# Optimization experiments

Hardware: AMD Instinct MI355X
Metric: run time of the kernel (lower is better)

The kernel has to match this reference:

```python
import jax, jax.numpy as jnp
import numpy as np

# Config (from ModelConfig in source; num_layers reduced to 4 for the reference)
B, T, D = 4, 8192, 1024
P = 512            # num_patches
S = 4              # patch_stride (OverlapAddDecoder upsample factor)
L = 4              # num transformer layers
NH, NKV, HD = 16, 4, 64
FF = 4096          # ffn_multiplier * D
KC = 256           # MoD capacity = 0.5 * P
V = 257            # vocab_size


def rmsnorm(x, w, eps=1e-6):
    return x * jax.lax.rsqrt(jnp.mean(x * x, -1, keepdims=True) + eps) * w


def rope_cache(n, d):
    theta = 1.0 / (10000.0 ** (jnp.arange(0, d, 2, dtype=jnp.float32) / d))
    fr = jnp.arange(n, dtype=jnp.float32)[:, None] * theta[None, :]
    e = jnp.concatenate([fr, fr], -1)
    return jnp.cos(e), jnp.sin(e)  # (n, d) each


def rot_half(x):
    h = x.shape[-1] // 2
    return jnp.concatenate([-x[..., h:], x[..., :h]], -1)


def setup_inputs() -> dict:
    key = jax.random.key(0)
    ks = iter(jax.random.split(key, 40))
    n = lambda s: jax.random.normal(next(ks), s, dtype=jnp.float32) * 0.02
    return {
        'tokens': jax.random.randint(next(ks), (B, T), 0, V),
        'emb': n((V, D)),
        'bp_w1': n((D // 2, D, 3)), 'bp_b1': jnp.zeros((D // 2,), jnp.float32),
        'bp_w2': n((1, D // 2, 3)), 'bp_b2': jnp.zeros((1,), jnp.float32),
        'enc_norm_w': jnp.ones((D,), jnp.float32),
        'router_w': n((L, D)),
        'ln1_w': jnp.ones((L, D), jnp.float32), 'ln2_w': jnp.ones((L, D), jnp.float32),
        'q_w': n((L, D, D)), 'k_w': n((L, D, NKV * HD)), 'v_w': n((L, D, NKV * HD)), 'o_w': n((L, D, D)),
        'gate_w': n((L, D, FF)), 'up_w': n((L, D, FF)), 'down_w': n((L, FF, D)),
        'dec_proj_w': n((D, S * D)), 'dec_proj_b': jnp.zeros((S * D,), jnp.float32),
        'dec_mlp_w1': n((D, D // 4)), 'dec_mlp_b1': jnp.zeros((D // 4,), jnp.float32),
        'dec_mlp_w2': n((D // 4, S)), 'dec_mlp_b2': jnp.zeros((S,), jnp.float32),
        'dec_norm_w': jnp.ones((D,), jnp.float32),
        'head_w': n((D, V)),
    }


def reference(tokens, emb, bp_w1, bp_b1, bp_w2, bp_b2, enc_norm_w, router_w,
              ln1_w, ln2_w, q_w, k_w, v_w, o_w, gate_w, up_w, down_w,
              dec_proj_w, dec_proj_b, dec_mlp_w1, dec_mlp_b1, dec_mlp_w2, dec_mlp_b2,
              dec_norm_w, head_w):
    x = emb[tokens]  # (B, T, D) byte embeddings

    # --- LearnedBoundaryPredictor: 2-layer 1D CNN -> per-segment soft boundaries ---
    dn = ('NCH', 'OIH', 'NCH')
    xT = x.transpose(0, 2, 1)  # (B, D, T)
    h1 = jax.lax.conv_general_dilated(xT, bp_w1, (1,), ((1, 1),), dimension_numbers=dn) + bp_b1[None, :, None]
    h1 = jax.nn.gelu(h1)
    lg = jax.lax.conv_general_dilated(h1, bp_w2, (1,), ((1, 1),), dimension_numbers=dn) + bp_b2[None, :, None]
    lg = lg[:, 0, :]  # (B, T)

    seg = T // P  # uniform segments (T divisible by P so all segments equal)
    lgw = jax.nn.softmax(lg.reshape(B, P, seg), -1)
    pos = jnp.arange(T, dtype=jnp.float32).reshape(P, seg)
    bp = jnp.sum(lgw * pos[None], -1)                                   # (B, P) soft boundary positions
    ent = -jnp.sum(lgw * jnp.log(jnp.clip(lgw, 1e-8)), -1) / np.log(seg)  # (B, P) entropy signal

    # --- gather patch embeddings at boundary positions, RMSNorm ---
    idx = jnp.clip(bp.astype(jnp.int32), 0, T - 1)
    patches = jnp.take_along_axis(x, idx[..., None], 1)  # (B, P, D)
    xp = rmsnorm(patches, enc_norm_w)

    cos, sin = rope_cache(P, HD)
    b_idx = jnp.arange(B)[:, None]
    causal = jnp.tril(jnp.ones((KC, KC), bool))
    G = NH // NKV

    # --- MoD-routed transformer stack: top-k tokens go through the layer ---
    for l in range(L):
        rl = jnp.einsum('bpd,d->bp', xp, router_w[l]) + ent  # router logits (entropy-boosted)
        _, sel = jax.lax.top_k(rl, KC)
        sel = jnp.sort(sel, -1)  # ascending positions -> causal order preserved
        xs = xp[b_idx, sel]      # (B, KC, D) selected tokens
        g = jax.nn.sigmoid(rl[b_idx, sel])[..., None]  # router gate
        cs = cos[sel][:, None]   # (B, 1, KC, HD)
        sn = sin[sel][:, None]

        # GQA with RoPE, causal
        h = rmsnorm(xs, ln1_w[l])
        q = (h @ q_w[l]).reshape(B, KC, NH, HD).transpose(0, 2, 1, 3)
        k = (h @ k_w[l]).reshape(B, KC, NKV, HD).transpose(0, 2, 1, 3)
        v = (h @ v_w[l]).reshape(B, KC, NKV, HD).transpose(0, 2, 1, 3)
        q = q * cs + rot_half(q) * sn
        k = k * cs + rot_half(k) * sn
        k = jnp.repeat(k, G, axis=1)
        v = jnp.repeat(v, G, axis=1)
        sc = jnp.einsum('bhqd,bhkd->bhqk', q, k) / np.sqrt(HD)
        sc = jnp.where(causal, sc, -1e30)
        a = jax.nn.softmax(sc, -1)
        ao = (jnp.einsum('bhqk,bhkd->bhqd', a, v).transpose(0, 2, 1, 3).reshape(B, KC, D)) @ o_w[l]

        x2 = xs + ao
        h2 = rmsnorm(x2, ln2_w[l])
        ff = (jax.nn.silu(h2 @ gate_w[l]) * (h2 @ up_w[l])) @ down_w[l]
        delta = ao + ff  # layer(x_sel) - x_sel
        xp = xp.at[b_idx, sel].add(g * delta)  # scatter back; unselected pass through

    # --- OverlapAddDecoder ---
    proj = (xp @ dec_proj_w + dec_proj_b).reshape(B, P, S, D)
    win = jax.nn.sigmoid(jax.nn.gelu(xp @ dec_mlp_w1 + dec_mlp_b1) @ dec_mlp_w2 + dec_mlp_b2)  # (B, P, S)
    out = rmsnorm((proj * win[..., None]).reshape(B, P * S, D), dec_norm_w)
    return out @ head_w  # (B, P*S, V) byte logits
```

## Files before the change

### kernel.cpp

```cpp
#include <hip/hip_runtime.h>
#include <hip/hip_bf16.h>
#include <math.h>

constexpr int Bn  = 4;
constexpr int Tn  = 8192;
constexpr int Dn  = 1024;
constexpr int Pn  = 512;
constexpr int SEGn= 16;
constexpr int Sn  = 4;
constexpr int Ln  = 4;
constexpr int NHn = 16;
constexpr int NKVn= 4;
constexpr int HDn = 64;
constexpr int FFn = 4096;
constexpr int KCn = 256;
constexpr int Vn  = 257;
constexpr int DHn = 512;

constexpr long OFF_EW  = 0;
constexpr long OFF_CA  = 394752;
constexpr long OFF_CB  = 427520;
constexpr long OFF_CC  = 460288;
constexpr long OFF_ENT = 493056;
constexpr long OFF_IDX = 495104;
constexpr long OFF_XP  = 497152;
constexpr long OFF_RL  = 2594304;
constexpr long OFF_SEL = 2596352;
constexpr long OFF_G   = 2597376;
constexpr long SCR     = 2598400;
constexpr long SC_XS   = 0;
constexpr long SC_H    = 1048576;
constexpr long SC_Q    = 2097152;
constexpr long SC_KV   = 3145728;
constexpr long SC_AOUT = 3670016;
constexpr long SC_AO   = 4718592;
constexpr long SC_H2   = 5767168;
constexpr long SC_GU   = 6815744;
constexpr long SC_FF   = 15204352;
constexpr long SC_PROJ = 0;
constexpr long SC_HMLP = 8388608;
constexpr long SC_WIN  = 8912896;
constexpr long SC_Y    = 8921088;
constexpr long SC_EA   = 0;
constexpr long SC_WB   = 524288;
constexpr long OFF_WT    = 19908096;
constexpr long OFF_PARTS = 24102400;
constexpr long OFF_GHL   = 28820992;

typedef __attribute__((ext_vector_type(8))) short short8;
typedef __attribute__((ext_vector_type(4))) float floatx4;

__device__ __forceinline__ float geluf(float x) {
    float u = 0.7978845608028654f * (x + 0.044715f * x * x * x);
    float e = __expf(2.f * u);
    float t = 1.f - 2.f / (e + 1.f);
    return 0.5f * x * (1.f + t);
}
__device__ __forceinline__ float sigmf(float x) { return 1.f / (1.f + expf(-x)); }

__device__ __forceinline__ void cvt_hilo(float x, unsigned short& h, unsigned short& l) {
    unsigned u = __float_as_uint(x);
    h = (unsigned short)(u >> 16);
    float r = x - __uint_as_float(u & 0xffff0000u);
    l = (unsigned short)(__float_as_uint(r) >> 16);
}

typedef const __attribute__((address_space(1))) unsigned int* gas_p;
typedef __attribute__((address_space(3))) unsigned int* las_p;
__device__ __forceinline__ void gload16(const unsigned short* g, unsigned short* l) {
    __builtin_amdgcn_global_load_lds((gas_p)g, (las_p)l, 16, 0, 0);
}

__device__ __forceinline__ float blk_sum256(float v, float* red) {
    for (int o = 32; o > 0; o >>= 1) v += __shfl_down(v, o);
    int lane = threadIdx.x & 63, w = threadIdx.x >> 6;
    if (lane == 0) red[w] = v;
    __syncthreads();
    float r = red[0] + red[1] + red[2] + red[3];
    __syncthreads();
    return r;
}

__global__ void k_emb_pad(const float* __restrict__ emb, unsigned short* __restrict__ EA) {
    int i = blockIdx.x * blockDim.x + threadIdx.x;
    if (i >= 384 * 1024) return;
    int r = i >> 10, d = i & 1023;
    float v = (r < Vn) ? emb[r * 1024 + d] : 0.f;
    unsigned short hh, ll;
    cvt_hilo(v, hh, ll);
    EA[(long)r * 2048 + d] = hh;
    EA[(long)r * 2048 + 1024 + d] = ll;
}

__global__ void k_wconv_w1(const float* __restrict__ w1, unsigned short* __restrict__ WB) {
    int i = blockIdx.x * blockDim.x + threadIdx.x;
    if (i >= 1536 * 1024) return;
    int n = i >> 10, k = i & 1023;
    float v = w1[(n / 3) * 3072 + k * 3 + (n % 3)];
    unsigned short hh, ll;
    cvt_hilo(v, hh, ll);
    WB[(long)n * 2048 + k] = hh;
    WB[(long)n * 2048 + 1024 + k] = ll;
}

__global__ void k_ewred(const float* __restrict__ parts, float* __restrict__ EW) {
    int i = blockIdx.x * blockDim.x + threadIdx.x;
    if (i >= 3 * Vn * DHn) return;
    int dk = i / (Vn * DHn);
    int rem = i - dk * (Vn * DHn);
    int v = rem >> 9, o = rem & 511;
    long src = (long)v * 1536 + o * 3 + dk;
    float s = 0.f;
    constexpr long MN = 384L * 1536;
    #pragma unroll
    for (int c = 0; c < 4; c++) s += parts[c * MN + src];
    EW[i] = s;
}

__global__ void k_conv1(const int* __restrict__ tok, const float* __restrict__ EW,
                        const float* __restrict__ b1, const float* __restrict__ w2,
                        float* __restrict__ cA, float* __restrict__ cB, float* __restrict__ cC) {
    int wave = threadIdx.x >> 6, lane = threadIdx.x & 63;
    int gidx = blockIdx.x * 4 + wave;
    int b = gidx / Tn, t = gidx - b * Tn;
    int tk  = tok[b * Tn + t];
    int tkm = (t > 0)      ? tok[b * Tn + t - 1] : -1;
    int tkp = (t < Tn - 1) ? tok[b * Tn + t + 1] : -1;
    const float* E0 = EW;
    const float* E1 = EW + (long)Vn * DHn;
    const float* E2 = EW + 2L * Vn * DHn;
    float a0 = 0.f, a1 = 0.f, a2 = 0.f;
    #pragma unroll
    for (int u = 0; u < DHn / 64; u++) {
        int o = lane + u * 64;
        float s = b1[o] + E1[tk * DHn + o];
        if (tkm >= 0) s += E0[tkm * DHn + o];
        if (tkp >= 0) s += E2[tkp * DHn + o];
        float hg = geluf(s);
        a0 += hg * w2[o * 3 + 0];
        a1 += hg * w2[o * 3 + 1];
        a2 += hg * w2[o * 3 + 2];
    }
    for (int o = 32; o > 0; o >>= 1) {
        a0 += __shfl_down(a0, o); a1 += __shfl_down(a1, o); a2 += __shfl_down(a2, o);
    }
    if (lane == 0) { cA[gidx] = a0; cB[gidx] = a1; cC[gidx] = a2; }
}

__global__ void k_patchstats(const float* __restrict__ cA, const float* __restrict__ cB,
                             const float* __restrict__ cC, const float* __restrict__ b2,
                             float* __restrict__ ent_out, int* __restrict__ idx_out) {
    int pid = blockIdx.x * blockDim.x + threadIdx.x;
    if (pid >= Bn * Pn) return;
    int b = pid / Pn, p = pid - b * Pn;
    float lgv[SEGn];
    float m = -3.4e38f;
    for (int s = 0; s < SEGn; s++) {
        int t = p * SEGn + s;
        float v = b2[0] + cB[b * Tn + t];
        if (t > 0)      v += cA[b * Tn + t - 1];
        if (t < Tn - 1) v += cC[b * Tn + t + 1];
        lgv[s] = v; m = fmaxf(m, v);
    }
    float Z = 0.f;
    for (int s = 0; s < SEGn; s++) { lgv[s] = expf(lgv[s] - m); Z += lgv[s]; }
    float inv = 1.f / Z;
    float bp = 0.f, en = 0.f;
    for (int s = 0; s < SEGn; s++) {
        float w = lgv[s] * inv;
        bp += w * (float)(p * SEGn + s);
        en -= w * logf(fmaxf(w, 1e-8f));
    }
    en *= (1.f / 2.772588722239781f);
    ent_out[pid] = en;
    int ix = (int)bp;
    ix = ix < 0 ? 0 : (ix > Tn - 1 ? Tn - 1 : ix);
    idx_out[pid] = ix;
}

__global__ void k_xp(const int* __restrict__ tok, const int* __restrict__ idx,
                     const float* __restrict__ emb, const float* __restrict__ nw,
                     float* __restrict__ xp) {
    int pid = blockIdx.x;
    int b = pid / Pn;
    int tk = tok[b * Tn + idx[pid]];
    const float* row = emb + (long)tk * Dn;
    __shared__ float red[4];
    float v[4]; float ss = 0.f;
    #pragma unroll
    for (int j = 0; j < 4; j++) { v[j] = row[threadIdx.x + j * 256]; ss += v[j] * v[j]; }
    ss = blk_sum256(ss, red);
    float sc = 1.f / sqrtf(ss * (1.f / Dn) + 1e-6f);
    #pragma unroll
    for (int j = 0; j < 4; j++) {
        int d = threadIdx.x + j * 256;
        xp[(long)pid * Dn + d] = v[j] * sc * nw[d];
    }
}

__global__ void k_router(const float* __restrict__ xp, const float* __restrict__ rw,
                         const float* __restrict__ ent, float* __restrict__ rl) {
    int pid = blockIdx.x;
    const float* xr = xp + (long)pid * Dn;
    __shared__ float red[4];
    float s = 0.f;
    #pragma unroll
    for (int j = 0; j < 4; j++) { int d = threadIdx.x + j * 256; s += xr[d] * rw[d]; }
    s = blk_sum256(s, red);
    if (threadIdx.x == 0) rl[pid] = s + ent[pid];
}

__global__ void k_topk(const float* __restrict__ rl, int* __restrict__ sel, float* __restrict__ g) {
    int b = blockIdx.x, p = threadIdx.x;
    __shared__ float vals[Pn];
    __shared__ int flag[Pn];
    float v = rl[b * Pn + p];
    vals[p] = v;
    __syncthreads();
    int rank = 0;
    for (int q = 0; q < Pn; q++) {
        float vq = vals[q];
        rank += (vq > v || (vq == v && q < p)) ? 1 : 0;
    }
    int selected = rank < KCn ? 1 : 0;
    flag[p] = selected;
    __syncthreads();
    if (selected) {
        int pos = 0;
        for (int q = 0; q < p; q++) pos += flag[q];
        sel[b * KCn + pos] = p;
        g[b * KCn + pos] = sigmf(v);
    }
}

__global__ void k_gather_ln1(const float* __restrict__ xp, const int* __restrict__ sel,
                             const float* __restrict__ w, float* __restrict__ xs,
                             unsigned short* __restrict__ hHL) {
    int r = blockIdx.x;
    int b = r / KCn;
    int p = sel[r];
    const float* src = xp + ((long)b * Pn + p) * Dn;
    __shared__ float red[4];
    float v[4]; float ss = 0.f;
    #pragma unroll
    for (int j = 0; j < 4; j++) { v[j] = src[threadIdx.x + j * 256]; ss += v[j] * v[j]; }
    ss = blk_sum256(ss, red);
    float sc = 1.f / sqrtf(ss * (1.f / Dn) + 1e-6f);
    #pragma unroll
    for (int j = 0; j < 4; j++) {
        int d = threadIdx.x + j * 256;
        xs[(long)r * Dn + d] = v[j];
        unsigned short hh, ll;
        cvt_hilo(v[j] * sc * w[d], hh, ll);
        hHL[(long)r * 2048 + d] = hh;
        hHL[(long)r * 2048 + 1024 + d] = ll;
    }
}

__global__ void k_wconv(const float* __restrict__ Wm, unsigned short* __restrict__ Whl,
                        int K, int N) {
    __shared__ float t[32][33];
    int n0 = blockIdx.x * 32, k0 = blockIdx.y * 32;
    int tx = threadIdx.x & 31, ty = threadIdx.x >> 5;
    #pragma unroll
    for (int r = 0; r < 4; r++) {
        int k = k0 + ty + 8 * r, n = n0 + tx;
        t[ty + 8 * r][tx] = (n < N) ? Wm[(long)k * N + n] : 0.f;
    }
    __syncthreads();
    long K2 = 2L * K;
    #pragma unroll
    for (int r = 0; r < 4; r++) {
        int n = n0 + ty + 8 * r, k = k0 + tx;
        float v = t[tx][ty + 8 * r];
        unsigned short hh, ll;
        cvt_hilo(v, hh, ll);
        Whl[(long)n * K2 + k] = hh;
        Whl[(long)n * K2 + K + k] = ll;
    }
}

__global__ void k_xcvt(const float* __restrict__ src, unsigned short* __restrict__ dhl, int n) {
    int i = blockIdx.x * blockDim.x + threadIdx.x;
    if (i >= n) return;
    int r = i >> 10, d = i & 1023;
    unsigned short hh, ll;
    cvt_hilo(src[i], hh, ll);
    dhl[(long)r * 2048 + d] = hh;
    dhl[(long)r * 2048 + 1024 + d] = ll;
}

__global__ __launch_bounds__(256, 2) void k_mfma3(
        const unsigned short* __restrict__ Ag, const unsigned short* __restrict__ Bg,
        float* __restrict__ Cmat, const float* __restrict__ bias,
        int M, int N, int K, int splitK, float* __restrict__ parts) {
    __shared__ alignas(16) unsigned short As[2][128 * 64], Bs[2][128 * 64];
    int tid = threadIdx.x;
    int m0 = blockIdx.y * 128, n0 = blockIdx.x * 128;
    int kc = blockIdx.z;
    int Kc = K / splitK, kbase = kc * Kc, KT = Kc >> 5;
    int lane = tid & 63, wid = tid >> 6;
    int wm = (wid & 1) * 64, wn = (wid >> 1) * 64;
    int quad = lane >> 4, l16 = lane & 15;

    int srow8 = lane >> 3;
    int spos  = lane & 7;
    int cch   = spos ^ srow8;
    long K2 = 2L * K;
    long coff = (cch < 4) ? (long)(cch * 8) : (long)K + (long)((cch - 4) * 8);
    const unsigned short* Aseg = Ag + (long)(m0 + srow8) * K2 + coff;
    const unsigned short* Bseg = Bg + (long)(n0 + srow8) * K2 + coff;

    floatx4 acc[4][4];
    #pragma unroll
    for (int i = 0; i < 4; i++)
        #pragma unroll
        for (int j = 0; j < 4; j++) acc[i][j] = (floatx4){0.f, 0.f, 0.f, 0.f};

    auto stagef = [&](unsigned short* Ad, unsigned short* Bd, long kb) {
        #pragma unroll
        for (int t = 0; t < 4; t++) {
            int sa = wid * 4 + t;
            gload16(Aseg + (long)sa * 8 * K2 + kb, Ad + sa * 512);
            gload16(Bseg + (long)sa * 8 * K2 + kb, Bd + sa * 512);
        }
    };

    int ph = quad ^ (l16 & 7);
    stagef(As[0], Bs[0], kbase);
    __syncthreads();
    int cur = 0;
    for (int ks = 0; ks < KT; ks++) {
        if (ks + 1 < KT)
            stagef(As[cur ^ 1], Bs[cur ^ 1], kbase + (long)(ks + 1) * 32);

        const unsigned short* Ac = As[cur];
        const unsigned short* Bc = Bs[cur];
        short8 ah[4], al2[4], bh[4], bl2[4];
        #pragma unroll
        for (int i = 0; i < 4; i++) {
            int r = wm + i * 16 + l16;
            ah[i]  = *(const short8*)&Ac[r * 64 + ph * 8];
            al2[i] = *(const short8*)&Ac[r * 64 + (ph ^ 4) * 8];
        }
        #pragma unroll
        for (int j = 0; j < 4; j++) {
            int c = wn + j * 16 + l16;
            bh[j]  = *(const short8*)&Bc[c * 64 + ph * 8];
            bl2[j] = *(const short8*)&Bc[c * 64 + (ph ^ 4) * 8];
        }
        #pragma unroll
        for (int i = 0; i < 4; i++)
            #pragma unroll
            for (int j = 0; j < 4; j++) {
                acc[i][j] = __builtin_amdgcn_mfma_f32_16x16x32_bf16(ah[i],  bh[j],  acc[i][j], 0, 0, 0);
                acc[i][j] = __builtin_amdgcn_mfma_f32_16x16x32_bf16(ah[i],  bl2[j], acc[i][j], 0, 0, 0);
                acc[i][j] = __builtin_amdgcn_mfma_f32_16x16x32_bf16(al2[i], bh[j],  acc[i][j], 0, 0, 0);
            }
        __syncthreads();
        cur ^= 1;
    }

    long MN = (long)M * N;
    #pragma unroll
    for (int j = 0; j < 4; j++) {
        int n = n0 + wn + j * 16 + l16;
        if (n >= N) continue;
        float bvx = bias ? bias[n] : 0.f;
        #pragma unroll
        for (int i = 0; i < 4; i++) {
            int mb = m0 + wm + i * 16 + quad * 4;
            #pragma unroll
            for (int r = 0; r < 4; r++) {
                if (splitK > 1) parts[kc * MN + (long)(mb + r) * N + n] = acc[i][j][r];
                else            Cmat[(long)(mb + r) * N + n] = acc[i][j][r] + bvx;
            }
        }
    }
}

__global__ void k_reduce(const float* __restrict__ parts, float* __restrict__ out,
                         const float* __restrict__ bias, long MN, int sk, int N) {
    long i = (long)blockIdx.x * blockDim.x + threadIdx.x;
    if (i >= MN) return;
    float s = 0.f;
    for (int c = 0; c < sk; c++) s += parts[c * MN + i];
    if (bias) s += bias[(int)(i % N)];
    out[i] = s;
}

__global__ void k_rope(float* __restrict__ buf, const int* __restrict__ sel, int nh, int stride) {
    int tid = blockIdx.x * blockDim.x + threadIdx.x;
    int total = Bn * KCn * nh * 32;
    if (tid >= total) return;
    int d = tid & 31;
    int h = (tid >> 5) % nh;
    int r = tid / (32 * nh);
    int pos = sel[r];
    float theta = powf(10000.f, -(float)(2 * d) / 64.f);
    float ang = (float)pos * theta;
    float c = cosf(ang), s = sinf(ang);
    long base = (long)r * stride + h * 64 + d;
    float x1 = buf[base], x2 = buf[base + 32];
    buf[base]      = x1 * c - x2 * s;
    buf[base + 32] = x2 * c + x1 * s;
}

constexpr int APS = 72;
__global__ __launch_bounds__(256) void k_attn(const float* __restrict__ q, const float* __restrict__ kv,
                       unsigned short* __restrict__ aoHL) {
    int bx = blockIdx.x, h = blockIdx.y, b = blockIdx.z;
    int hk = h >> 2;
    int qb0 = bx * 64;
    int tid = threadIdx.x, lane = tid & 63, wid = tid >> 6;
    int quad = lane >> 4, l16 = lane & 15;
    __shared__ alignas(16) unsigned short LdsA[9216], LdsB[9216];
    unsigned short* Kh = LdsA;          unsigned short* Kl = LdsB;
    unsigned short* Ph = LdsA;          unsigned short* Pl = LdsB;
    unsigned short* Vth = LdsA + 4608;  unsigned short* Vtl = LdsB + 4608;

    int qrow = qb0 + wid * 16 + l16;
    short8 qh[2], ql[2];
    #pragma unroll
    for (int ks = 0; ks < 2; ks++) {
        const float* qp = q + ((long)(b * KCn + qrow)) * (NHn * HDn) + h * HDn + ks * 32 + quad * 8;
        float tmp[8];
        *(float4*)tmp = *(const float4*)qp;
        *(float4*)(tmp + 4) = *(const float4*)(qp + 4);
        #pragma unroll
        for (int j = 0; j < 8; j++) {
            unsigned short hh, ll;
            cvt_hilo(tmp[j], hh, ll);
            qh[ks][j] = (short)hh; ql[ks][j] = (short)ll;
        }
    }

    floatx4 sacc[16];
    #pragma unroll
    for (int t = 0; t < 16; t++) sacc[t] = (floatx4){0.f, 0.f, 0.f, 0.f};

    int qmax = qb0 + 63;
    int nkc = qmax / 128 + 1;
    for (int kc = 0; kc < nkc; kc++) {
        __syncthreads();
        {
            int r = tid >> 1, dh = (tid & 1) * 32;
            const float* kp = kv + ((long)(b * KCn + kc * 128 + r)) * 512 + hk * HDn + dh;
            #pragma unroll
            for (int f = 0; f < 8; f++) {
                float tmp[4];
                *(float4*)tmp = *(const float4*)(kp + f * 4);
                unsigned short h0, h1, h2, h3, l0, l1, l2, l3;
                cvt_hilo(tmp[0], h0, l0); cvt_hilo(tmp[1], h1, l1);
                cvt_hilo(tmp[2], h2, l2); cvt_hilo(tmp[3], h3, l3);
                *(ushort4*)&Kh[r * APS + dh + f * 4] = make_ushort4(h0, h1, h2, h3);
                *(ushort4*)&Kl[r * APS + dh + f * 4] = make_ushort4(l0, l1, l2, l3);
            }
        }
        __syncthreads();
        #pragma unroll
        for (int tj = 0; tj < 8; tj++) {
            int kr = tj * 16 + l16;
            int gt = kc * 8 + tj;
            #pragma unroll
            for (int ks = 0; ks < 2; ks++) {
                short8 bh0 = *(const short8*)&Kh[kr * APS + ks * 32 + quad * 8];
                short8 bl0 = *(const short8*)&Kl[kr * APS + ks * 32 + quad * 8];
                sacc[gt] = __builtin_amdgcn_mfma_f32_16x16x32_bf16(qh[ks], bh0, sacc[gt], 0, 0, 0);
                sacc[gt] = __builtin_amdgcn_mfma_f32_16x16x32_bf16(qh[ks], bl0, sacc[gt], 0, 0, 0);
                sacc[gt] = __builtin_amdgcn_mfma_f32_16x16x32_bf16(ql[ks], bh0, sacc[gt], 0, 0, 0);
            }
        }
    }

    float rowinv[4];
    #pragma unroll
    for (int r = 0; r < 4; r++) {
        int qg = qb0 + wid * 16 + quad * 4 + r;
        float mm = -3.4e38f;
        #pragma unroll
        for (int t = 0; t < 16; t++) {
            int key = t * 16 + l16;
            float s = (key <= qg) ? sacc[t][r] * 0.125f : -1e30f;
            sacc[t][r] = s;
            mm = fmaxf(mm, s);
        }
        #pragma unroll
        for (int o = 1; o < 16; o <<= 1) mm = fmaxf(mm, __shfl_xor(mm, o));
        float zz = 0.f;
        #pragma unroll
        for (int t = 0; t < 16; t++) {
            float e = expf(sacc[t][r] - mm);
            sacc[t][r] = e; zz += e;
        }
        #pragma unroll
        for (int o = 1; o < 16; o <<= 1) zz += __shfl_xor(zz, o);
        rowinv[r] = 1.f / zz;
    }

    floatx4 oacc[4];
    #pragma unroll
    for (int dt = 0; dt < 4; dt++) oacc[dt] = (floatx4){0.f, 0.f, 0.f, 0.f};
    int npv = qmax / 64 + 1;
    for (int c4 = 0; c4 < npv; c4++) {
        __syncthreads();
        {
            #pragma unroll
            for (int it = 0; it < 4; it++) {
                int task = tid + 256 * it;
                int kloc = task & 63, d4 = (task >> 6) * 4;
                float tmp[4];
                *(float4*)tmp = *(const float4*)(kv + ((long)(b * KCn + c4 * 64 + kloc)) * 512 + 256 + hk * HDn + d4);
                #pragma unroll
                for (int i = 0; i < 4; i++) {
                    unsigned short hh, ll;
                    cvt_hilo(tmp[i], hh, ll);
                    Vth[(d4 + i) * APS + kloc] = hh;
                    Vtl[(d4 + i) * APS + kloc] = ll;
                }
            }
        }
        #pragma unroll
        for (int tt = 0; tt < 4; tt++) {
            int t = c4 * 4 + tt;
            #pragma unroll
            for (int r = 0; r < 4; r++) {
                int row = wid * 16 + quad * 4 + r;
                float pv2 = sacc[t][r] * rowinv[r];
                unsigned short hh, ll;
                cvt_hilo(pv2, hh, ll);
                Ph[row * APS + tt * 16 + l16] = hh;
                Pl[row * APS + tt * 16 + l16] = ll;
            }
        }
        __syncthreads();
        short8 pah[2], pal[2];
        #pragma unroll
        for (int ks = 0; ks < 2; ks++) {
            pah[ks] = *(const short8*)&Ph[(wid * 16 + l16) * APS + ks * 32 + quad * 8];
            pal[ks] = *(const short8*)&Pl[(wid * 16 + l16) * APS + ks * 32 + quad * 8];
        }
        #pragma unroll
        for (int dt = 0; dt < 4; dt++) {
            #pragma unroll
            for (int ks = 0; ks < 2; ks++) {
                short8 vbh = *(const short8*)&Vth[(dt * 16 + l16) * APS + ks * 32 + quad * 8];
                short8 vbl = *(const short8*)&Vtl[(dt * 16 + l16) * APS + ks * 32 + quad * 8];
                oacc[dt] = __builtin_amdgcn_mfma_f32_16x16x32_bf16(pah[ks], vbh, oacc[dt], 0, 0, 0);
                oacc[dt] = __builtin_amdgcn_mfma_f32_16x16x32_bf16(pah[ks], vbl, oacc[dt], 0, 0, 0);
                oacc[dt] = __builtin_amdgcn_mfma_f32_16x16x32_bf16(pal[ks], vbh, oacc[dt], 0, 0, 0);
            }
        }
    }

    #pragma unroll
    for (int dt = 0; dt < 4; dt++) {
        #pragma unroll
        for (int r = 0; r < 4; r++) {
            int row = qb0 + wid * 16 + quad * 4 + r;
            long base = ((long)(b * KCn + row)) * 2048 + h * HDn + dt * 16 + l16;
            unsigned short hh, ll;
            cvt_hilo(oacc[dt][r], hh, ll);
            aoHL[base] = hh; aoHL[base + 1024] = ll;
        }
    }
}

__global__ void k_add_ln2(const float* __restrict__ xs, const float* __restrict__ ao,
                          const float* __restrict__ w, unsigned short* __restrict__ h2HL) {
    int r = blockIdx.x;
    __shared__ float red[4];
    float v[4]; float ss = 0.f;
    #pragma unroll
    for (int j = 0; j < 4; j++) {
        int d = threadIdx.x + j * 256;
        float x = xs[(long)r * Dn + d] + ao[(long)r * Dn + d];
        v[j] = x; ss += x * x;
    }
    ss = blk_sum256(ss, red);
    float sc = 1.f / sqrtf(ss * (1.f / Dn) + 1e-6f);
    #pragma unroll
    for (int j = 0; j < 4; j++) {
        int d = threadIdx.x + j * 256;
        unsigned short hh, ll;
        cvt_hilo(v[j] * sc * w[d], hh, ll);
        h2HL[(long)r * 2048 + d] = hh;
        h2HL[(long)r * 2048 + 1024 + d] = ll;
    }
}

__global__ void k_silu_mul(const float* __restrict__ C, unsigned short* __restrict__ ghl, int n) {
    int i = blockIdx.x * blockDim.x + threadIdx.x;
    if (i < n) {
        int r = i >> 12, c = i & 4095;
        float x = C[(long)r * 8192 + c];
        float u = C[(long)r * 8192 + 4096 + c];
        unsigned short hh, ll;
        cvt_hilo(x * sigmf(x) * u, hh, ll);
        ghl[(long)r * 8192 + c] = hh;
        ghl[(long)r * 8192 + 4096 + c] = ll;
    }
}

__global__ void k_scatter(float* __restrict__ xp, const float* __restrict__ ao,
                          const float* __restrict__ ff, const float* __restrict__ g,
                          const int* __restrict__ sel) {
    int r = blockIdx.x;
    int b = r / KCn;
    int p = sel[r];
    float gg = g[r];
    float* dst = xp + ((long)b * Pn + p) * Dn;
    #pragma unroll
    for (int j = 0; j < 4; j++) {
        int d = threadIdx.x + j * 256;
        dst[d] += gg * (ao[(long)r * Dn + d] + ff[(long)r * Dn + d]);
    }
}

__global__ void k_win(const float* __restrict__ hmlp, const float* __restrict__ w2,
                      const float* __restrict__ b2, float* __restrict__ win) {
    int tid = blockIdx.x * blockDim.x + threadIdx.x;
    if (tid >= Bn * Pn * Sn) return;
    int s = tid & 3; int r = tid >> 2;
    float acc = b2[s];
    const float* hr = hmlp + (long)r * 256;
    for (int i = 0; i < 256; i++) acc += geluf(hr[i]) * w2[i * 4 + s];
    win[tid] = sigmf(acc);
}

__global__ void k_dec_norm(const float* __restrict__ proj, const float* __restrict__ win,
                           const float* __restrict__ w, unsigned short* __restrict__ yHL) {
    int r = blockIdx.x;
    float wv = win[r];
    __shared__ float red[4];
    float v[4]; float ss = 0.f;
    #pragma unroll
    for (int j = 0; j < 4; j++) {
        int d = threadIdx.x + j * 256;
        float x = proj[(long)r * Dn + d] * wv;
        v[j] = x; ss += x * x;
    }
    ss = blk_sum256(ss, red);
    float sc = 1.f / sqrtf(ss * (1.f / Dn) + 1e-6f);
    #pragma unroll
    for (int j = 0; j < 4; j++) {
        int d = threadIdx.x + j * 256;
        unsigned short hh, ll;
        cvt_hilo(v[j] * sc * w[d], hh, ll);
        yHL[(long)r * 2048 + d] = hh;
        yHL[(long)r * 2048 + 1024 + d] = ll;
    }
}

extern "C" void kernel_launch(void* const* d_in, const int* in_sizes, int n_in,
                              void* d_out, int out_size, void* d_ws, size_t ws_size,
                              hipStream_t stream) {
    const int*   tokens     = (const int*)  d_in[0];
    const float* emb        = (const float*)d_in[1];
    const float* bp_w1      = (const float*)d_in[2];
    const float* bp_b1      = (const float*)d_in[3];
    const float* bp_w2      = (const float*)d_in[4];
    const float* bp_b2      = (const float*)d_in[5];
    const float* enc_norm_w = (const float*)d_in[6];
    const float* router_w   = (const float*)d_in[7];
    const float* ln1_w      = (const float*)d_in[8];
    const float* ln2_w      = (const float*)d_in[9];
    const float* q_w        = (const float*)d_in[10];
    const float* k_w        = (const float*)d_in[11];
    const float* v_w        = (const float*)d_in[12];
    const float* o_w        = (const float*)d_in[13];
    const float* gate_w     = (const float*)d_in[14];
    const float* up_w       = (const float*)d_in[15];
    const float* down_w     = (const float*)d_in[16];
    const float* dec_proj_w = (const float*)d_in[17];
    const float* dec_proj_b = (const float*)d_in[18];
    const float* dec_mlp_w1 = (const float*)d_in[19];
    const float* dec_mlp_b1 = (const float*)d_in[20];
    const float* dec_mlp_w2 = (const float*)d_in[21];
    const float* dec_mlp_b2 = (const float*)d_in[22];
    const float* dec_norm_w = (const float*)d_in[23];
    const float* head_w     = (const float*)d_in[24];
    float* out = (float*)d_out;

    float* W = (float*)d_ws;
    float* EW   = W + OFF_EW;
    float* cA   = W + OFF_CA;
    float* cB   = W + OFF_CB;
    float* cC   = W + OFF_CC;
    float* ent  = W + OFF_ENT;
    int*   idxb = (int*)(W + OFF_IDX);
    float* xp   = W + OFF_XP;
    float* rl   = W + OFF_RL;
    int*   sel  = (int*)(W + OFF_SEL);
    float* g    = W + OFF_G;
    float* scr  = W + SCR;
    float* xs   = scr + SC_XS;
    unsigned short* hHL   = (unsigned short*)(scr + SC_H);
    float* qb   = scr + SC_Q;
    float* kvb  = scr + SC_KV;
    unsigned short* aoutHL = (unsigned short*)(scr + SC_AOUT);
    float* ao   = scr + SC_AO;
    unsigned short* h2HL  = (unsigned short*)(scr + SC_H2);
    float* gupC = scr + SC_GU;
    float* ffb  = scr + SC_FF;
    float* proj = scr + SC_PROJ;
    float* hmlp = scr + SC_HMLP;
    float* win  = scr + SC_WIN;
    unsigned short* yHL   = (unsigned short*)(scr + SC_Y);
    unsigned short* EA    = (unsigned short*)(scr + SC_EA);
    unsigned short* WB    = (unsigned short*)(scr + SC_WB);
    unsigned short* WHL   = (unsigned short*)(W + OFF_WT);
    float* parts = W + OFF_PARTS;
    unsigned short* ghHL  = (unsigned short*)(W + OFF_GHL);
    unsigned short* xpHL  = (unsigned short*)(W + OFF_GHL);

    k_emb_pad<<<1536, 256, 0, stream>>>(emb, EA);
    k_wconv_w1<<<6144, 256, 0, stream>>>(bp_w1, WB);
    k_mfma3<<<dim3(12, 3, 4), 256, 0, stream>>>(EA, WB, nullptr, nullptr, 384, 1536, 1024, 4, parts);
    k_ewred<<<1542, 256, 0, stream>>>(parts, EW);
    k_conv1<<<Bn * Tn / 4, 256, 0, stream>>>(tokens, EW, bp_b1, bp_w2, cA, cB, cC);
    k_patchstats<<<(Bn * Pn + 255) / 256, 256, 0, stream>>>(cA, cB, cC, bp_b2, ent, idxb);
    k_xp<<<Bn * Pn, 256, 0, stream>>>(tokens, idxb, emb, enc_norm_w, xp);

    for (int l = 0; l < Ln; l++) {
        k_router<<<Bn * Pn, 256, 0, stream>>>(xp, router_w + (long)l * Dn, ent, rl);
        k_topk<<<Bn, Pn, 0, stream>>>(rl, sel, g);
        k_gather_ln1<<<Bn * KCn, 256, 0, stream>>>(xp, sel, ln1_w + (long)l * Dn, xs, hHL);

        k_wconv<<<dim3(32, 32), 256, 0, stream>>>(q_w + (long)l * Dn * Dn, WHL, 1024, 1024);
        k_mfma3<<<dim3(8, 8, 4), 256, 0, stream>>>(hHL, WHL, nullptr, nullptr, 1024, 1024, 1024, 4, parts);
        k_reduce<<<4096, 256, 0, stream>>>(parts, qb, nullptr, 1048576, 4, 1024);

        k_wconv<<<dim3(8, 32), 256, 0, stream>>>(k_w + (long)l * Dn * 256, WHL, 1024, 256);
        k_wconv<<<dim3(8, 32), 256, 0, stream>>>(v_w + (long)l * Dn * 256, WHL + 256L * 2048, 1024, 256);
        k_mfma3<<<dim3(4, 8, 8), 256, 0, stream>>>(hHL, WHL, nullptr, nullptr, 1024, 512, 1024, 8, parts);
        k_reduce<<<2048, 256, 0, stream>>>(parts, kvb, nullptr, 524288, 8, 512);

        k_rope<<<(Bn * KCn * NHn * 32 + 255) / 256, 256, 0, stream>>>(qb, sel, NHn, 1024);
        k_rope<<<(Bn * KCn * NKVn * 32 + 255) / 256, 256, 0, stream>>>(kvb, sel, NKVn, 512);
        k_attn<<<dim3(4, NHn, Bn), 256, 0, stream>>>(qb, kvb, aoutHL);

        k_wconv<<<dim3(32, 32), 256, 0, stream>>>(o_w + (long)l * Dn * Dn, WHL, 1024, 1024);
        k_mfma3<<<dim3(8, 8, 4), 256, 0, stream>>>(aoutHL, WHL, nullptr, nullptr, 1024, 1024, 1024, 4, parts);
        k_reduce<<<4096, 256, 0, stream>>>(parts, ao, nullptr, 1048576, 4, 1024);

        k_add_ln2<<<Bn * KCn, 256, 0, stream>>>(xs, ao, ln2_w + (long)l * Dn, h2HL);

        k_wconv<<<dim3(128, 32), 256, 0, stream>>>(gate_w + (long)l * Dn * FFn, WHL, 1024, 4096);
        k_wconv<<<dim3(128, 32), 256, 0, stream>>>(up_w + (long)l * Dn * FFn, WHL + 4096L * 2048, 1024, 4096);
        k_mfma3<<<dim3(64, 8, 1), 256, 0, stream>>>(h2HL, WHL, gupC, nullptr, 1024, 8192, 1024, 1, parts);

        k_silu_mul<<<(Bn * KCn * FFn + 255) / 256, 256, 0, stream>>>(gupC, ghHL, Bn * KCn * FFn);

        k_wconv<<<dim3(32, 128), 256, 0, stream>>>(down_w + (long)l * FFn * Dn, WHL, 4096, 1024);
        k_mfma3<<<dim3(8, 8, 4), 256, 0, stream>>>(ghHL, WHL, nullptr, nullptr, 1024, 1024, 4096, 4, parts);
        k_reduce<<<4096, 256, 0, stream>>>(parts, ffb, nullptr, 1048576, 4, 1024);

        k_scatter<<<Bn * KCn, 256, 0, stream>>>(xp, ao, ffb, g, sel);
    }

    k_xcvt<<<8192, 256, 0, stream>>>(xp, xpHL, 2097152);
    k_wconv<<<dim3(128, 32), 256, 0, stream>>>(dec_proj_w, WHL, 1024, 4096);
    k_mfma3<<<dim3(32, 16, 1), 256, 0, stream>>>(xpHL, WHL, proj, dec_proj_b, 2048, 4096, 1024, 1, parts);
    k_wconv<<<dim3(8, 32), 256, 0, stream>>>(dec_mlp_w1, WHL, 1024, 256);
    k_mfma3<<<dim3(2, 16, 4), 256, 0, stream>>>(xpHL, WHL, nullptr, nullptr, 2048, 256, 1024, 4, parts);
    k_reduce<<<2048, 256, 0, stream>>>(parts, hmlp, dec_mlp_b1, 524288, 4, 256);
    k_win<<<(Bn * Pn * Sn + 255) / 256, 256, 0, stream>>>(hmlp, dec_mlp_w2, dec_mlp_b2, win);
    k_dec_norm<<<Bn * Pn * Sn, 256, 0, stream>>>(proj, win, dec_norm_w, yHL);
    k_wconv<<<dim3(9, 32), 256, 0, stream>>>(head_w, WHL, 1024, 257);
    k_mfma3<<<dim3(3, 64, 2), 256, 0, stream>>>(yHL, WHL, nullptr, nullptr, 8192, 257, 1024, 2, parts);
    k_reduce<<<8224, 256, 0, stream>>>(parts, out, nullptr, 2105344, 2, 257);
}
```

Measured before the change: 1.607 ms.

## Fuse QKV projection, fold split-K reductions into consumers, merge decoder GEMMs

Concatenates the Q, K and V weight conversions and GEMMs into a single 1536-wide GEMM with split-K 2, and uses one finish kernel that reduces the partials and applies RoPE. The split-K reductions for the o-projection and down-projection move into the add+LN2 and scatter kernels. Gate and up weight conversion becomes one launch, and the decoder projection and MLP first layer share one GEMM with concatenated bias, with the window MLP folded into the decoder norm. Together these cut kernel launches and intermediate global round-trips, at the cost of a changed split-K schedule for the QKV GEMM.

```diff
diff --git a/kernel.cpp b/kernel.cpp
--- a/kernel.cpp
+++ b/kernel.cpp
@@ -30,21 +30,18 @@
 constexpr long SCR     = 2598400;
 constexpr long SC_XS   = 0;
 constexpr long SC_H    = 1048576;
-constexpr long SC_Q    = 2097152;
-constexpr long SC_KV   = 3145728;
+constexpr long SC_QKV  = 2097152;
 constexpr long SC_AOUT = 3670016;
 constexpr long SC_AO   = 4718592;
 constexpr long SC_H2   = 5767168;
 constexpr long SC_GU   = 6815744;
-constexpr long SC_FF   = 15204352;
 constexpr long SC_PROJ = 0;
-constexpr long SC_HMLP = 8388608;
-constexpr long SC_WIN  = 8912896;
 constexpr long SC_Y    = 8921088;
 constexpr long SC_EA   = 0;
 constexpr long SC_WB   = 524288;
 constexpr long OFF_WT    = 19908096;
 constexpr long OFF_PARTS = 24102400;
+constexpr long OFF_BIASC = OFF_PARTS + 4500000;
 constexpr long OFF_GHL   = 28820992;
 
 typedef __attribute__((ext_vector_type(8))) short short8;
@@ -257,10 +254,10 @@
     }
 }
 
-__global__ void k_wconv(const float* __restrict__ Wm, unsigned short* __restrict__ Whl,
-                        int K, int N) {
+__device__ __forceinline__ void wconv_body(const float* __restrict__ Wm,
+                                           unsigned short* __restrict__ Whl,
+                                           int K, int N, int roff, int n0, int k0) {
     __shared__ float t[32][33];
-    int n0 = blockIdx.x * 32, k0 = blockIdx.y * 32;
     int tx = threadIdx.x & 31, ty = threadIdx.x >> 5;
     #pragma unroll
     for (int r = 0; r < 4; r++) {
@@ -275,9 +272,34 @@
         float v = t[tx][ty + 8 * r];
         unsigned short hh, ll;
         cvt_hilo(v, hh, ll);
-        Whl[(long)n * K2 + k] = hh;
-        Whl[(long)n * K2 + K + k] = ll;
-    }
+        Whl[(long)(roff + n) * K2 + k] = hh;
+        Whl[(long)(roff + n) * K2 + K + k] = ll;
+    }
+}
+
+__global__ void k_wconv(const float* __restrict__ Wm, unsigned short* __restrict__ Whl,
+                        int K, int N, int roff) {
+    wconv_body(Wm, Whl, K, N, roff, blockIdx.x * 32, blockIdx.y * 32);
+}
+
+__global__ void k_wconv2(const float* __restrict__ Wa, const float* __restrict__ Wb,
+                         unsigned short* __restrict__ Whl, int K, int Nh) {
+    int nb = Nh >> 5;
+    int bx = blockIdx.x;
+    const float* src = (bx < nb) ? Wa : Wb;
+    int xb = (bx < nb) ? bx : bx - nb;
+    int roff = (bx < nb) ? 0 : Nh;
+    wconv_body(src, Whl, K, Nh, roff, xb * 32, blockIdx.y * 32);
+}
+
+__global__ void k_wconv_qkv(const float* __restrict__ qw, const float* __restrict__ kw,
+                            const float* __restrict__ vw, unsigned short* __restrict__ Whl) {
+    int bx = blockIdx.x;
+    const float* src; int xb, roff, Nsrc;
+    if (bx < 32)      { src = qw; xb = bx;      roff = 0;    Nsrc = 1024; }
+    else if (bx < 40) { src = kw; xb = bx - 32; roff = 1024; Nsrc = 256; }
+    else              { src = vw; xb = bx - 40; roff = 1280; Nsrc = 256; }
+    wconv_body(src, Whl, 1024, Nsrc, roff, xb * 32, blockIdx.y * 32);
 }
 
 __global__ void k_xcvt(const float* __restrict__ src, unsigned short* __restrict__ dhl, int n) {
@@ -389,25 +411,32 @@
     out[i] = s;
 }
 
-__global__ void k_rope(float* __restrict__ buf, const int* __restrict__ sel, int nh, int stride) {
-    int tid = blockIdx.x * blockDim.x + threadIdx.x;
-    int total = Bn * KCn * nh * 32;
-    if (tid >= total) return;
-    int d = tid & 31;
-    int h = (tid >> 5) % nh;
-    int r = tid / (32 * nh);
+__global__ void k_qkv_finish(const float* __restrict__ parts, const int* __restrict__ sel,
+                             float* __restrict__ qkv) {
+    int r = blockIdx.x;
     int pos = sel[r];
-    float theta = powf(10000.f, -(float)(2 * d) / 64.f);
-    float ang = (float)pos * theta;
-    float c = cosf(ang), s = sinf(ang);
-    long base = (long)r * stride + h * 64 + d;
-    float x1 = buf[base], x2 = buf[base + 32];
-    buf[base]      = x1 * c - x2 * s;
-    buf[base + 32] = x2 * c + x1 * s;
+    constexpr long MN = 1024L * 1536;
+    #pragma unroll
+    for (int it = 0; it < 3; it++) {
+        int pp = threadIdx.x + it * 256;
+        int head = pp >> 5, d = pp & 31;
+        long c1 = (long)r * 1536 + head * 64 + d;
+        float s1 = parts[c1] + parts[MN + c1];
+        float s2 = parts[c1 + 32] + parts[MN + c1 + 32];
+        if (head < 20) {
+            float theta = powf(10000.f, -(float)(2 * d) / 64.f);
+            float ang = (float)pos * theta;
+            float cc = cosf(ang), ssn = sinf(ang);
+            qkv[c1]      = s1 * cc - s2 * ssn;
+            qkv[c1 + 32] = s2 * cc + s1 * ssn;
+        } else {
+            qkv[c1] = s1; qkv[c1 + 32] = s2;
+        }
+    }
 }
 
 constexpr int APS = 72;
-__global__ __launch_bounds__(256) void k_attn(const float* __restrict__ q, const float* __restrict__ kv,
+__global__ __launch_bounds__(256) void k_attn(const float* __restrict__ qkv,
                        unsigned short* __restrict__ aoHL) {
     int bx = blockIdx.x, h = blockIdx.y, b = blockIdx.z;
     int hk = h >> 2;
@@ -423,7 +452,7 @@
     short8 qh[2], ql[2];
     #pragma unroll
     for (int ks = 0; ks < 2; ks++) {
-        const float* qp = q + ((long)(b * KCn + qrow)) * (NHn * HDn) + h * HDn + ks * 32 + quad * 8;
+        const float* qp = qkv + ((long)(b * KCn + qrow)) * 1536 + h * HDn + ks * 32 + quad * 8;
         float tmp[8];
         *(float4*)tmp = *(const float4*)qp;
         *(float4*)(tmp + 4) = *(const float4*)(qp + 4);
@@ -445,7 +474,7 @@
         __syncthreads();
         {
             int r = tid >> 1, dh = (tid & 1) * 32;
-            const float* kp = kv + ((long)(b * KCn + kc * 128 + r)) * 512 + hk * HDn + dh;
+            const float* kp = qkv + ((long)(b * KCn + kc * 128 + r)) * 1536 + 1024 + hk * HDn + dh;
             #pragma unroll
             for (int f = 0; f < 8; f++) {
                 float tmp[4];
@@ -510,7 +539,7 @@
                 int task = tid + 256 * it;
                 int kloc = task & 63, d4 = (task >> 6) * 4;
                 float tmp[4];
-                *(float4*)tmp = *(const float4*)(kv + ((long)(b * KCn + c4 * 64 + kloc)) * 512 + 256 + hk * HDn + d4);
+                *(float4*)tmp = *(const float4*)(qkv + ((long)(b * KCn + c4 * 64 + kloc)) * 1536 + 1280 + hk * HDn + d4);
                 #pragma unroll
                 for (int i = 0; i < 4; i++) {
                     unsigned short hh, ll;
@@ -566,15 +595,22 @@
     }
 }
 
-__global__ void k_add_ln2(const float* __restrict__ xs, const float* __restrict__ ao,
-                          const float* __restrict__ w, unsigned short* __restrict__ h2HL) {
+__global__ void k_add_ln2_red(const float* __restrict__ parts, const float* __restrict__ xs,
+                              const float* __restrict__ w, float* __restrict__ ao,
+                              unsigned short* __restrict__ h2HL) {
     int r = blockIdx.x;
+    constexpr long MN = 1024L * 1024;
     __shared__ float red[4];
     float v[4]; float ss = 0.f;
     #pragma unroll
     for (int j = 0; j < 4; j++) {
         int d = threadIdx.x + j * 256;
-        float x = xs[(long)r * Dn + d] + ao[(long)r * Dn + d];
+        long i = (long)r * Dn + d;
+        float a = 0.f;
+        #pragma unroll
+        for (int c = 0; c < 4; c++) a += parts[c * MN + i];
+        ao[i] = a;
+        float x = xs[i] + a;
         v[j] = x; ss += x * x;
     }
     ss = blk_sum256(ss, red);
@@ -602,42 +638,48 @@
     }
 }
 
-__global__ void k_scatter(float* __restrict__ xp, const float* __restrict__ ao,
-                          const float* __restrict__ ff, const float* __restrict__ g,
-                          const int* __restrict__ sel) {
+__global__ void k_scatter_red(float* __restrict__ xp, const float* __restrict__ ao,
+                              const float* __restrict__ parts, const float* __restrict__ g,
+                              const int* __restrict__ sel) {
     int r = blockIdx.x;
     int b = r / KCn;
     int p = sel[r];
     float gg = g[r];
+    constexpr long MN = 1024L * 1024;
     float* dst = xp + ((long)b * Pn + p) * Dn;
     #pragma unroll
     for (int j = 0; j < 4; j++) {
         int d = threadIdx.x + j * 256;
-        dst[d] += gg * (ao[(long)r * Dn + d] + ff[(long)r * Dn + d]);
-    }
-}
-
-__global__ void k_win(const float* __restrict__ hmlp, const float* __restrict__ w2,
-                      const float* __restrict__ b2, float* __restrict__ win) {
-    int tid = blockIdx.x * blockDim.x + threadIdx.x;
-    if (tid >= Bn * Pn * Sn) return;
-    int s = tid & 3; int r = tid >> 2;
-    float acc = b2[s];
-    const float* hr = hmlp + (long)r * 256;
-    for (int i = 0; i < 256; i++) acc += geluf(hr[i]) * w2[i * 4 + s];
-    win[tid] = sigmf(acc);
-}
-
-__global__ void k_dec_norm(const float* __restrict__ proj, const float* __restrict__ win,
-                           const float* __restrict__ w, unsigned short* __restrict__ yHL) {
+        long i = (long)r * Dn + d;
+        float f = 0.f;
+        #pragma unroll
+        for (int c = 0; c < 4; c++) f += parts[c * MN + i];
+        dst[d] += gg * (ao[i] + f);
+    }
+}
+
+__global__ void k_catbias(const float* __restrict__ a, const float* __restrict__ b,
+                          float* __restrict__ o) {
+    int i = blockIdx.x * blockDim.x + threadIdx.x;
+    if (i < 4352) o[i] = (i < 4096) ? a[i] : b[i - 4096];
+}
+
+__global__ void k_dec_norm_win(const float* __restrict__ projC, const float* __restrict__ w2,
+                               const float* __restrict__ b2, const float* __restrict__ w,
+                               unsigned short* __restrict__ yHL) {
     int r = blockIdx.x;
-    float wv = win[r];
+    int bp = r >> 2, s = r & 3;
     __shared__ float red[4];
+    const float* hr = projC + (long)bp * 4352 + 4096;
+    float acc = geluf(hr[threadIdx.x]) * w2[threadIdx.x * 4 + s];
+    acc = blk_sum256(acc, red);
+    float wv = sigmf(acc + b2[s]);
+    const float* pr = projC + (long)bp * 4352 + s * 1024;
     float v[4]; float ss = 0.f;
     #pragma unroll
     for (int j = 0; j < 4; j++) {
         int d = threadIdx.x + j * 256;
-        float x = proj[(long)r * Dn + d] * wv;
+        float x = pr[d] * wv;
         v[j] = x; ss += x * x;
     }
     ss = blk_sum256(ss, red);
@@ -696,21 +738,18 @@
     float* scr  = W + SCR;
     float* xs   = scr + SC_XS;
     unsigned short* hHL   = (unsigned short*)(scr + SC_H);
-    float* qb   = scr + SC_Q;
-    float* kvb  = scr + SC_KV;
+    float* qkv  = scr + SC_QKV;
     unsigned short* aoutHL = (unsigned short*)(scr + SC_AOUT);
     float* ao   = scr + SC_AO;
     unsigned short* h2HL  = (unsigned short*)(scr + SC_H2);
     float* gupC = scr + SC_GU;
-    float* ffb  = scr + SC_FF;
-    float* proj = scr + SC_PROJ;
-    float* hmlp = scr + SC_HMLP;
-    float* win  = scr + SC_WIN;
+    float* projC= scr + SC_PROJ;
     unsigned short* yHL   = (unsigned short*)(scr + SC_Y);
     unsigned short* EA    = (unsigned short*)(scr + SC_EA);
     unsigned short* WB    = (unsigned short*)(scr + SC_WB);
     unsigned short* WHL   = (unsigned short*)(W + OFF_WT);
     float* parts = W + OFF_PARTS;
+    float* biasc = W + OFF_BIASC;
     unsigned short* ghHL  = (unsigned short*)(W + OFF_GHL);
     unsigned short* xpHL  = (unsigned short*)(W + OFF_GHL);
 
@@ -727,47 +766,36 @@
         k_topk<<<Bn, Pn, 0, stream>>>(rl, sel, g);
         k_gather_ln1<<<Bn * KCn, 256, 0, stream>>>(xp, sel, ln1_w + (long)l * Dn, xs, hHL);
 
-        k_wconv<<<dim3(32, 32), 256, 0, stream>>>(q_w + (long)l * Dn * Dn, WHL, 1024, 1024);
-        k_mfma3<<<dim3(8, 8, 4), 256, 0, stream>>>(hHL, WHL, nullptr, nullptr, 1024, 1024, 1024, 4, parts);
-        k_reduce<<<4096, 256, 0, stream>>>(parts, qb, nullptr, 1048576, 4, 1024);
-
-        k_wconv<<<dim3(8, 32), 256, 0, stream>>>(k_w + (long)l * Dn * 256, WHL, 1024, 256);
-        k_wconv<<<dim3(8, 32), 256, 0, stream>>>(v_w + (long)l * Dn * 256, WHL + 256L * 2048, 1024, 256);
-        k_mfma3<<<dim3(4, 8, 8), 256, 0, stream>>>(hHL, WHL, nullptr, nullptr, 1024, 512, 1024, 8, parts);
-        k_reduce<<<2048, 256, 0, stream>>>(parts, kvb, nullptr, 524288, 8, 512);
-
-        k_rope<<<(Bn * KCn * NHn * 32 + 255) / 256, 256, 0, stream>>>(qb, sel, NHn, 1024);
-        k_rope<<<(Bn * KCn * NKVn * 32 + 255) / 256, 256, 0, stream>>>(kvb, sel, NKVn, 512);
-        k_attn<<<dim3(4, NHn, Bn), 256, 0, stream>>>(qb, kvb, aoutHL);
-
-        k_wconv<<<dim3(32, 32), 256, 0, stream>>>(o_w + (long)l * Dn * Dn, WHL, 1024, 1024);
+        k_wconv_qkv<<<dim3(48, 32), 256, 0, stream>>>(q_w + (long)l * Dn * Dn,
+                                                      k_w + (long)l * Dn * 256,
+                                                      v_w + (long)l * Dn * 256, WHL);
+        k_mfma3<<<dim3(12, 8, 2), 256, 0, stream>>>(hHL, WHL, nullptr, nullptr, 1024, 1536, 1024, 2, parts);
+        k_qkv_finish<<<Bn * KCn, 256, 0, stream>>>(parts, sel, qkv);
+
+        k_attn<<<dim3(4, NHn, Bn), 256, 0, stream>>>(qkv, aoutHL);
+
+        k_wconv<<<dim3(32, 32), 256, 0, stream>>>(o_w + (long)l * Dn * Dn, WHL, 1024, 1024, 0);
         k_mfma3<<<dim3(8, 8, 4), 256, 0, stream>>>(aoutHL, WHL, nullptr, nullptr, 1024, 1024, 1024, 4, parts);
-        k_reduce<<<4096, 256, 0, stream>>>(parts, ao, nullptr, 1048576, 4, 1024);
-
-        k_add_ln2<<<Bn * KCn, 256, 0, stream>>>(xs, ao, ln2_w + (long)l * Dn, h2HL);
-
-        k_wconv<<<dim3(128, 32), 256, 0, stream>>>(gate_w + (long)l * Dn * FFn, WHL, 1024, 4096);
-        k_wconv<<<dim3(128, 32), 256, 0, stream>>>(up_w + (long)l * Dn * FFn, WHL + 4096L * 2048, 1024, 4096);
+        k_add_ln2_red<<<Bn * KCn, 256, 0, stream>>>(parts, xs, ln2_w + (long)l * Dn, ao, h2HL);
+
+        k_wconv2<<<dim3(256, 32), 256, 0, stream>>>(gate_w + (long)l * Dn * FFn,
+                                                    up_w + (long)l * Dn * FFn, WHL, 1024, 4096);
         k_mfma3<<<dim3(64, 8, 1), 256, 0, stream>>>(h2HL, WHL, gupC, nullptr, 1024, 8192, 1024, 1, parts);
 
         k_silu_mul<<<(Bn * KCn * FFn + 255) / 256, 256, 0, stream>>>(gupC, ghHL, Bn * KCn * FFn);
 
-        k_wconv<<<dim3(32, 128), 256, 0, stream>>>(down_w + (long)l * FFn * Dn, WHL, 4096, 1024);
+        k_wconv<<<dim3(32, 128), 256, 0, stream>>>(down_w + (long)l * FFn * Dn, WHL, 4096, 1024, 0);
         k_mfma3<<<dim3(8, 8, 4), 256, 0, stream>>>(ghHL, WHL, nullptr, nullptr, 1024, 1024, 4096, 4, parts);
-        k_reduce<<<4096, 256, 0, stream>>>(parts, ffb, nullptr, 1048576, 4, 1024);
-
-        k_scatter<<<Bn * KCn, 256, 0, stream>>>(xp, ao, ffb, g, sel);
+        k_scatter_red<<<Bn * KCn, 256, 0, stream>>>(xp, ao, parts, g, sel);
     }
 
     k_xcvt<<<8192, 256, 0, stream>>>(xp, xpHL, 2097152);
-    k_wconv<<<dim3(128, 32), 256, 0, stream>>>(dec_proj_w, WHL, 1024, 4096);
-    k_mfma3<<<dim3(32, 16, 1), 256, 0, stream>>>(xpHL, WHL, proj, dec_proj_b, 2048, 4096, 1024, 1, parts);
-    k_wconv<<<dim3(8, 32), 256, 0, stream>>>(dec_mlp_w1, WHL, 1024, 256);
-    k_mfma3<<<dim3(2, 16, 4), 256, 0, stream>>>(xpHL, WHL, nullptr, nullptr, 2048, 256, 1024, 4, parts);
-    k_reduce<<<2048, 256, 0, stream>>>(parts, hmlp, dec_mlp_b1, 524288, 4, 256);
-    k_win<<<(Bn * Pn * Sn + 255) / 256, 256, 0, stream>>>(hmlp, dec_mlp_w2, dec_mlp_b2, win);
-    k_dec_norm<<<Bn * Pn * Sn, 256, 0, stream>>>(proj, win, dec_norm_w, yHL);
-    k_wconv<<<dim3(9, 32), 256, 0, stream>>>(head_w, WHL, 1024, 257);
+    k_catbias<<<17, 256, 0, stream>>>(dec_proj_b, dec_mlp_b1, biasc);
+    k_wconv<<<dim3(128, 32), 256, 0, stream>>>(dec_proj_w, WHL, 1024, 4096, 0);
+    k_wconv<<<dim3(8, 32), 256, 0, stream>>>(dec_mlp_w1, WHL, 1024, 256, 4096);
+    k_mfma3<<<dim3(34, 16, 1), 256, 0, stream>>>(xpHL, WHL, projC, biasc, 2048, 4352, 1024, 1, parts);
+    k_dec_norm_win<<<Bn * Pn * Sn, 256, 0, stream>>>(projC, dec_mlp_w2, dec_mlp_b2, dec_norm_w, yHL);
+    k_wconv<<<dim3(9, 32), 256, 0, stream>>>(head_w, WHL, 1024, 257, 0);
     k_mfma3<<<dim3(3, 64, 2), 256, 0, stream>>>(yHL, WHL, nullptr, nullptr, 8192, 257, 1024, 2, parts);
     k_reduce<<<8224, 256, 0, stream>>>(parts, out, nullptr, 2105344, 2, 257);
 }
```

Measured after the change: 1.456 ms. -9.4%, faster.
